# Optimization experiments

Hardware: AMD Instinct MI355X
Metric: run time of the kernel (lower is better)

## Reference

```python
import jax, jax.numpy as jnp
import numpy as np

HIDDEN = 2880
NUM_HEADS = 64
NUM_KV_HEADS = 8
HEAD_DIM = 64
ROPE_THETA = 150000.0
WINDOW = 128  # sliding window size (attend to last WINDOW tokens incl. current)
SCALE = HEAD_DIM ** -0.5
Q_SIZE = NUM_HEADS * HEAD_DIM          # 4096
KV_SIZE = NUM_KV_HEADS * HEAD_DIM      # 512


def _rope_neox(x, positions):
    # x: [T, n_heads, HEAD_DIM]; neox-style rotary over the full head dim
    half = HEAD_DIM // 2
    inv_freq = 1.0 / (ROPE_THETA ** (jnp.arange(half, dtype=jnp.float32) / half))
    freqs = positions.astype(jnp.float32)[:, None] * inv_freq[None, :]  # [T, half]
    cos = jnp.cos(freqs)[:, None, :]
    sin = jnp.sin(freqs)[:, None, :]
    x1, x2 = x[..., :half], x[..., half:]
    return jnp.concatenate([x1 * cos - x2 * sin, x2 * cos + x1 * sin], axis=-1)


def setup_inputs() -> dict:
    key = jax.random.key(0)
    k1, k2, k3, k4 = jax.random.split(key, 4)
    T = 2048
    hidden_states = jax.random.normal(k1, (T, HIDDEN), dtype=jnp.float32)
    positions = jnp.arange(T, dtype=jnp.int32)
    w_qkv = jax.random.normal(k2, (HIDDEN, Q_SIZE + 2 * KV_SIZE), dtype=jnp.float32) * (HIDDEN ** -0.5)
    w_o = jax.random.normal(k3, (Q_SIZE, HIDDEN), dtype=jnp.float32) * (Q_SIZE ** -0.5)
    sinks = jax.random.normal(k4, (NUM_HEADS,), dtype=jnp.float32)
    return {"positions": positions, "hidden_states": hidden_states,
            "w_qkv": w_qkv, "w_o": w_o, "sinks": sinks}


def reference(positions, hidden_states, w_qkv, w_o, sinks):
    T = hidden_states.shape[0]
    qkv = hidden_states @ w_qkv  # [T, 5120]
    q = qkv[:, :Q_SIZE].reshape(T, NUM_HEADS, HEAD_DIM)
    k = qkv[:, Q_SIZE:Q_SIZE + KV_SIZE].reshape(T, NUM_KV_HEADS, HEAD_DIM)
    v = qkv[:, Q_SIZE + KV_SIZE:].reshape(T, NUM_KV_HEADS, HEAD_DIM)

    q = _rope_neox(q, positions)
    k = _rope_neox(k, positions)

    # GQA: each group of NUM_HEADS//NUM_KV_HEADS query heads shares one kv head
    rep = NUM_HEADS // NUM_KV_HEADS
    k = jnp.repeat(k, rep, axis=1)  # [T, NUM_HEADS, HEAD_DIM]
    v = jnp.repeat(v, rep, axis=1)

    scores = jnp.einsum('qhd,khd->hqk', q, k) * SCALE  # [H, T, T]
    pos_q = positions[:, None]
    pos_k = positions[None, :]
    mask = (pos_k <= pos_q) & (pos_q - pos_k < WINDOW)  # causal + sliding window
    neg = jnp.finfo(scores.dtype).min
    scores = jnp.where(mask[None, :, :], scores, neg)

    # softmax with per-head learned sink logit included in the denominator
    m = jnp.maximum(scores.max(axis=-1), sinks[:, None])      # [H, T]
    e = jnp.exp(scores - m[..., None])                        # [H, T, T]
    denom = e.sum(axis=-1) + jnp.exp(sinks[:, None] - m)      # [H, T]
    probs = e / denom[..., None]

    attn = jnp.einsum('hqk,khd->qhd', probs, v).reshape(T, Q_SIZE)
    return attn @ w_o  # [T, HIDDEN]
```

## Files before the change

kernel.cpp:

```cpp
#include <hip/hip_runtime.h>
#include <hip/hip_bf16.h>

#define T_SEQ   2048
#define HIDDEN  2880
#define NQ      64
#define NKV     8
#define HD      64
#define QSIZE   4096
#define KVSIZE  512
#define QKV_N   5120
#define WINDOW  128
#define SCALE_F 0.125f
#define ROPE_L2 0.53733241958f

typedef unsigned short u16;
typedef __attribute__((ext_vector_type(8))) short short8;
typedef __attribute__((ext_vector_type(4))) float f32x4;

__device__ __forceinline__ u16 f2bf(float f) {
  __hip_bfloat16 b = __float2bfloat16(f);
  u16 u; __builtin_memcpy(&u, &b, 2); return u;
}

__device__ __forceinline__ void gload16(const u16* g, u16* l) {
  __builtin_amdgcn_global_load_lds(
      (const __attribute__((address_space(1))) void*)g,
      (__attribute__((address_space(3))) void*)l, 16, 0, 0);
}

#define CAST_BLKS 5760
#define TQ_BX 160
#define TQ_BLKS (160 * 45)
#define TO_BX 90
#define TO_BLKS (90 * 64)
#define PREP_BLKS (CAST_BLKS + TQ_BLKS + TO_BLKS)

__global__ void prep_kernel(const float* __restrict__ hidden,
                            const float* __restrict__ w_qkv,
                            const float* __restrict__ w_o,
                            u16* __restrict__ Xb, u16* __restrict__ Wqt,
                            u16* __restrict__ Wot) {
  __shared__ float tile[32][65];
  const int b = blockIdx.x, tid = threadIdx.x;
  if (b < CAST_BLKS) {
    int i = b * 256 + tid;
    float4 v = ((const float4*)hidden)[i];
    ushort4 o;
    o.x = f2bf(v.x); o.y = f2bf(v.y); o.z = f2bf(v.z); o.w = f2bf(v.w);
    ((ushort4*)Xb)[i] = o;
    return;
  }
  const float* in; u16* out; int R, C, bx, by;
  if (b < CAST_BLKS + TQ_BLKS) {
    int bb = b - CAST_BLKS; bx = bb % TQ_BX; by = bb / TQ_BX;
    in = w_qkv; out = Wqt; R = HIDDEN; C = QKV_N;
  } else {
    int bb = b - CAST_BLKS - TQ_BLKS; bx = bb % TO_BX; by = bb / TO_BX;
    in = w_o; out = Wot; R = QSIZE; C = HIDDEN;
  }
  const int r0 = by * 64, c0 = bx * 32;
  const int tx = tid & 31, ty = tid >> 5;
#pragma unroll
  for (int i = 0; i < 64; i += 8)
    tile[tx][ty + i] = in[(size_t)(r0 + ty + i) * C + c0 + tx];
  __syncthreads();
  const int tx2 = tid & 63, ty2 = tid >> 6;
#pragma unroll
  for (int i = 0; i < 32; i += 4)
    out[(size_t)(c0 + ty2 + i) * R + r0 + tx2] = f2bf(tile[ty2 + i][tx2]);
}

template <int MODE>
__global__ __launch_bounds__(256)
void gemm_bt_kernel(const u16* __restrict__ A, const u16* __restrict__ B,
                    float* __restrict__ Cout, const int* __restrict__ positions,
                    u16* __restrict__ qb, u16* __restrict__ kb,
                    u16* __restrict__ vb, int K, int Bvalid, int Nout, int ldc) {
  __shared__ __align__(16) u16 As[128 * 64];
  __shared__ __align__(16) u16 Bs[128 * 64];
  const int tid = threadIdx.x;
  const int lane = tid & 63, wave = tid >> 6;
  const int quad = lane >> 4, l16 = lane & 15;
  const int wm = wave >> 1, wn = wave & 1;
  const int m0 = blockIdx.x * 128, n0 = blockIdx.y * 128;

  const u16* Aptr[4]; const u16* Bptr[4]; u16* Alds[4]; u16* Blds[4];
#pragma unroll
  for (int it = 0; it < 4; ++it) {
    int c = it * 256 + tid;
    int r = c >> 3;
    int lcol = ((c & 7) ^ (r & 7)) * 8;
    Aptr[it] = A + (size_t)(m0 + r) * K + lcol;
    int br = n0 + r; br = br < Bvalid ? br : Bvalid - 1;
    Bptr[it] = B + (size_t)br * K + lcol;
    Alds[it] = As + c * 8;
    Blds[it] = Bs + c * 8;
  }

  f32x4 acc[4][4] = {};
  const int sw0 = (quad ^ (l16 & 7)) * 8;

  for (int kt = 0; kt < K; kt += 64) {
#pragma unroll
    for (int it = 0; it < 4; ++it) gload16(Aptr[it] + kt, Alds[it]);
#pragma unroll
    for (int it = 0; it < 4; ++it) gload16(Bptr[it] + kt, Blds[it]);
    asm volatile("s_waitcnt vmcnt(0)" ::: "memory");
    __syncthreads();
#pragma unroll
    for (int kk = 0; kk < 2; ++kk) {
      const int swo = sw0 ^ (kk * 32);
      short8 af[4], bf[4];
#pragma unroll
      for (int i = 0; i < 4; ++i)
        af[i] = *(const short8*)(As + (wm * 64 + i * 16 + l16) * 64 + swo);
#pragma unroll
      for (int j = 0; j < 4; ++j)
        bf[j] = *(const short8*)(Bs + (wn * 64 + j * 16 + l16) * 64 + swo);
#pragma unroll
      for (int i = 0; i < 4; ++i)
#pragma unroll
        for (int j = 0; j < 4; ++j)
          acc[i][j] = __builtin_amdgcn_mfma_f32_16x16x32_bf16(af[i], bf[j], acc[i][j], 0, 0, 0);
    }
    __syncthreads();
  }

  if (MODE == 0) {
#pragma unroll
    for (int i = 0; i < 4; ++i) {
      const int row = m0 + wm * 64 + i * 16 + quad * 4;
#pragma unroll
      for (int j = 0; j < 4; ++j) {
        const int col = n0 + wn * 64 + j * 16 + l16;
        if (col < Nout)
#pragma unroll
          for (int r = 0; r < 4; ++r)
            Cout[(size_t)(row + r) * ldc + col] = acc[i][j][r];
      }
    }
  } else {
    const int region = (n0 < QSIZE) ? 0 : (n0 < QSIZE + KVSIZE ? 1 : 2);
    if (region <= 1) {
      float invs[2];
#pragma unroll
      for (int j = 0; j < 2; ++j)
        invs[j] = exp2f(-(float)(j * 16 + l16) * ROPE_L2);
#pragma unroll
      for (int i = 0; i < 4; ++i) {
#pragma unroll
        for (int r = 0; r < 4; ++r) {
          const int row = m0 + wm * 64 + i * 16 + quad * 4 + r;
          const float pos = (float)positions[row];
#pragma unroll
          for (int j = 0; j < 2; ++j) {
            float s, c;
            sincosf(pos * invs[j], &s, &c);
            const float x1 = acc[i][j][r], x2 = acc[i][j + 2][r];
            const float o1 = x1 * c - x2 * s, o2 = x2 * c + x1 * s;
            const int col = n0 + wn * 64 + j * 16 + l16;
            if (region == 0) {
              qb[(size_t)row * QSIZE + col] = f2bf(o1);
              qb[(size_t)row * QSIZE + col + 32] = f2bf(o2);
            } else {
              kb[(size_t)row * KVSIZE + col - QSIZE] = f2bf(o1);
              kb[(size_t)row * KVSIZE + col - QSIZE + 32] = f2bf(o2);
            }
          }
        }
      }
    } else {
#pragma unroll
      for (int i = 0; i < 4; ++i) {
        const int row = m0 + wm * 64 + i * 16 + quad * 4;
#pragma unroll
        for (int j = 0; j < 4; ++j) {
          const int col = n0 + wn * 64 + j * 16 + l16 - (QSIZE + KVSIZE);
#pragma unroll
          for (int r = 0; r < 4; ++r)
            vb[(size_t)(row + r) * KVSIZE + col] = f2bf(acc[i][j][r]);
        }
      }
    }
  }
}

__global__ __launch_bounds__(256, 2)
void attn_kernel(const u16* __restrict__ qb, const u16* __restrict__ kb,
                 const u16* __restrict__ vb, const float* __restrict__ sinks,
                 u16* __restrict__ attnb) {
  __shared__ __align__(16) u16 Ks[160 * 72];
  __shared__ __align__(16) u16 Vt[64 * 164];
  __shared__ __align__(16) u16 Pb[4 * 16 * 164];
  const int qt = blockIdx.x, g = blockIdx.y;
  const int q0 = qt * 32, kstart = q0 - 128;
  const int tid = threadIdx.x;
  const int lane = tid & 63, wave = tid >> 6;
  const int quad = lane >> 4, l16 = lane & 15;

  for (int s = tid; s < 1280; s += 256) {
    int r = s >> 3, c8 = (s & 7) * 8;
    int tg = kstart + r; tg = tg < 0 ? 0 : tg;
    *(short8*)(Ks + r * 72 + c8) =
        *(const short8*)(kb + (size_t)tg * KVSIZE + g * HD + c8);
  }
  {
    const u16* vbase = vb + g * HD;
#pragma unroll
    for (int it = 0; it < 5; ++it) {
      int s = it * 256 + tid;
      int r = s >> 3, c8 = (s & 7) * 8;
      int tg = kstart + r; tg = tg < 0 ? 0 : tg;
      gload16(vbase + (size_t)tg * KVSIZE + c8, Pb + s * 8);
    }
  }
  asm volatile("s_waitcnt vmcnt(0)" ::: "memory");
  __syncthreads();

  short8 bk[10][2];
#pragma unroll
  for (int jf = 0; jf < 10; ++jf)
#pragma unroll
    for (int kk = 0; kk < 2; ++kk)
      bk[jf][kk] = *(const short8*)(Ks + (jf * 16 + l16) * 72 + kk * 32 + quad * 8);

  for (int s = tid; s < 1280; s += 256) {
    int k8 = s >> 6, d = s & 63;
    short8 tmp;
#pragma unroll
    for (int j = 0; j < 8; ++j) tmp[j] = (short)Pb[(k8 * 8 + j) * 64 + d];
    *(short8*)(Vt + d * 164 + k8 * 8) = tmp;
  }
  __syncthreads();

  const int strip = wave & 1, hb = wave >> 1;
  const int qrow0 = q0 + strip * 16;
  u16* Pw = Pb + wave * 16 * 164;
  for (int hh = 0; hh < 4; ++hh) {
    const int h = g * 8 + hb + hh * 2;
    short8 aq[2];
#pragma unroll
    for (int kk = 0; kk < 2; ++kk)
      aq[kk] = *(const short8*)(qb + (size_t)(qrow0 + l16) * QSIZE + h * HD + kk * 32 + quad * 8);
    f32x4 sc[10];
#pragma unroll
    for (int jf = 0; jf < 10; ++jf) {
      f32x4 c = {0.f, 0.f, 0.f, 0.f};
#pragma unroll
      for (int kk = 0; kk < 2; ++kk)
        c = __builtin_amdgcn_mfma_f32_16x16x32_bf16(aq[kk], bk[jf][kk], c, 0, 0, 0);
      sc[jf] = c;
    }

    const float sink = sinks[h];
    float pinv[4];
#pragma unroll
    for (int r = 0; r < 4; ++r) {
      const int qg = qrow0 + quad * 4 + r;
      float mx = -3.0e38f;
#pragma unroll
      for (int jf = 0; jf < 10; ++jf) {
        int kg = kstart + jf * 16 + l16;
        bool valid = (kg >= 0) && (kg <= qg) && (qg - kg < WINDOW);
        float sv = valid ? sc[jf][r] * SCALE_F : -3.0e38f;
        sc[jf][r] = sv;
        mx = fmaxf(mx, sv);
      }
#pragma unroll
      for (int d = 1; d < 16; d <<= 1) mx = fmaxf(mx, __shfl_xor(mx, d, 64));
      mx = fmaxf(mx, sink);
      float sum = 0.f;
#pragma unroll
      for (int jf = 0; jf < 10; ++jf) {
        float e = __expf(sc[jf][r] - mx);
        sc[jf][r] = e;
        sum += e;
      }
#pragma unroll
      for (int d = 1; d < 16; d <<= 1) sum += __shfl_xor(sum, d, 64);
      sum += __expf(sink - mx);
      pinv[r] = 1.0f / sum;
    }

#pragma unroll
    for (int jf = 0; jf < 10; ++jf)
#pragma unroll
      for (int r = 0; r < 4; ++r)
        Pw[(quad * 4 + r) * 164 + jf * 16 + l16] = f2bf(sc[jf][r] * pinv[r]);

    f32x4 o[4] = {};
#pragma unroll
    for (int kk = 0; kk < 5; ++kk) {
      short8 ap = *(const short8*)(Pw + l16 * 164 + kk * 32 + quad * 8);
#pragma unroll
      for (int jf = 0; jf < 4; ++jf) {
        short8 bv = *(const short8*)(Vt + (jf * 16 + l16) * 164 + kk * 32 + quad * 8);
        o[jf] = __builtin_amdgcn_mfma_f32_16x16x32_bf16(ap, bv, o[jf], 0, 0, 0);
      }
    }
#pragma unroll
    for (int jf = 0; jf < 4; ++jf)
#pragma unroll
      for (int r = 0; r < 4; ++r) {
        int qg = qrow0 + quad * 4 + r;
        attnb[(size_t)qg * QSIZE + h * HD + jf * 16 + l16] = f2bf(o[jf][r]);
      }
  }
}

extern "C" void kernel_launch(void* const* d_in, const int* in_sizes, int n_in,
                              void* d_out, int out_size, void* d_ws, size_t ws_size,
                              hipStream_t stream) {
  (void)in_sizes; (void)n_in; (void)out_size; (void)ws_size;
  const int*   positions = (const int*)d_in[0];
  const float* hidden    = (const float*)d_in[1];
  const float* w_qkv     = (const float*)d_in[2];
  const float* w_o       = (const float*)d_in[3];
  const float* sinks     = (const float*)d_in[4];

  char* p = (char*)d_ws;
  u16* Xb    = (u16*)p; p += (size_t)T_SEQ * HIDDEN * 2;
  u16* Wqt   = (u16*)p; p += (size_t)QKV_N * HIDDEN * 2;
  u16* Wot   = (u16*)p; p += (size_t)HIDDEN * QSIZE * 2;
  u16* qb    = (u16*)p; p += (size_t)T_SEQ * QSIZE * 2;
  u16* kb    = (u16*)p; p += (size_t)T_SEQ * KVSIZE * 2;
  u16* vb    = (u16*)p; p += (size_t)T_SEQ * KVSIZE * 2;
  u16* attnb = (u16*)p; p += (size_t)T_SEQ * QSIZE * 2;

  prep_kernel<<<PREP_BLKS, 256, 0, stream>>>(hidden, w_qkv, w_o, Xb, Wqt, Wot);
  gemm_bt_kernel<1><<<dim3(T_SEQ / 128, QKV_N / 128), 256, 0, stream>>>(
      Xb, Wqt, nullptr, positions, qb, kb, vb, HIDDEN, QKV_N, QKV_N, QKV_N);
  attn_kernel<<<dim3(T_SEQ / 32, NKV), 256, 0, stream>>>(qb, kb, vb, sinks, attnb);
  gemm_bt_kernel<0><<<dim3(T_SEQ / 128, 23), 256, 0, stream>>>(
      attnb, Wot, (float*)d_out, nullptr, nullptr, nullptr, nullptr,
      QSIZE, HIDDEN, HIDDEN, HIDDEN);
}
```

Baseline: 343.0 us.

## Double-buffer GEMM LDS tiles and remap blocks by XCD for L2 reuse

```diff
diff --git a/kernel.cpp b/kernel.cpp
--- a/kernel.cpp
+++ b/kernel.cpp
@@ -71,20 +71,28 @@
 }
 
 template <int MODE>
-__global__ __launch_bounds__(256)
+__global__ __launch_bounds__(256, 2)
 void gemm_bt_kernel(const u16* __restrict__ A, const u16* __restrict__ B,
                     float* __restrict__ Cout, const int* __restrict__ positions,
                     u16* __restrict__ qb, u16* __restrict__ kb,
-                    u16* __restrict__ vb, int K, int Bvalid, int Nout, int ldc) {
-  __shared__ __align__(16) u16 As[128 * 64];
-  __shared__ __align__(16) u16 Bs[128 * 64];
+                    u16* __restrict__ vb, int K, int NKT, int Bvalid, int Nout,
+                    int ldc, int NX, int NYC, int NY) {
+  __shared__ __align__(16) u16 As[2][128 * 64];
+  __shared__ __align__(16) u16 Bs[2][128 * 64];
+  const int bb = blockIdx.x;
+  const int xcd = bb & 7, bi = bb >> 3;
+  const int ny = xcd * NYC + (bi % NYC);
+  const int mx = bi / NYC;
+  if (ny >= NY || mx >= NX) return;
+  const int m0 = mx * 128, n0 = ny * 128;
+
   const int tid = threadIdx.x;
   const int lane = tid & 63, wave = tid >> 6;
   const int quad = lane >> 4, l16 = lane & 15;
   const int wm = wave >> 1, wn = wave & 1;
-  const int m0 = blockIdx.x * 128, n0 = blockIdx.y * 128;
-
-  const u16* Aptr[4]; const u16* Bptr[4]; u16* Alds[4]; u16* Blds[4];
+
+  const u16* Aptr[4]; const u16* Bptr[4];
+  u16* Al[2][4]; u16* Bl[2][4];
 #pragma unroll
   for (int it = 0; it < 4; ++it) {
     int c = it * 256 + tid;
@@ -93,37 +101,67 @@
     Aptr[it] = A + (size_t)(m0 + r) * K + lcol;
     int br = n0 + r; br = br < Bvalid ? br : Bvalid - 1;
     Bptr[it] = B + (size_t)br * K + lcol;
-    Alds[it] = As + c * 8;
-    Blds[it] = Bs + c * 8;
+    Al[0][it] = &As[0][c * 8]; Al[1][it] = &As[1][c * 8];
+    Bl[0][it] = &Bs[0][c * 8]; Bl[1][it] = &Bs[1][c * 8];
   }
 
   f32x4 acc[4][4] = {};
   const int sw0 = (quad ^ (l16 & 7)) * 8;
 
-  for (int kt = 0; kt < K; kt += 64) {
-#pragma unroll
-    for (int it = 0; it < 4; ++it) gload16(Aptr[it] + kt, Alds[it]);
-#pragma unroll
-    for (int it = 0; it < 4; ++it) gload16(Bptr[it] + kt, Blds[it]);
-    asm volatile("s_waitcnt vmcnt(0)" ::: "memory");
-    __syncthreads();
+#pragma unroll
+  for (int it = 0; it < 4; ++it) gload16(Aptr[it], Al[0][it]);
+#pragma unroll
+  for (int it = 0; it < 4; ++it) gload16(Bptr[it], Bl[0][it]);
+
+  int kt = 64;
+  for (int t = 0; t < NKT - 1; ++t, kt += 64) {
+    const int cur = t & 1, nxt = cur ^ 1;
+#pragma unroll
+    for (int it = 0; it < 4; ++it) gload16(Aptr[it] + kt, Al[nxt][it]);
+#pragma unroll
+    for (int it = 0; it < 4; ++it) gload16(Bptr[it] + kt, Bl[nxt][it]);
+    asm volatile("s_waitcnt vmcnt(8)\n\ts_barrier" ::: "memory");
+    const u16* Ab = &As[cur][0];
+    const u16* Bb = &Bs[cur][0];
 #pragma unroll
     for (int kk = 0; kk < 2; ++kk) {
       const int swo = sw0 ^ (kk * 32);
       short8 af[4], bf[4];
 #pragma unroll
       for (int i = 0; i < 4; ++i)
-        af[i] = *(const short8*)(As + (wm * 64 + i * 16 + l16) * 64 + swo);
+        af[i] = *(const short8*)(Ab + (wm * 64 + i * 16 + l16) * 64 + swo);
 #pragma unroll
       for (int j = 0; j < 4; ++j)
-        bf[j] = *(const short8*)(Bs + (wn * 64 + j * 16 + l16) * 64 + swo);
+        bf[j] = *(const short8*)(Bb + (wn * 64 + j * 16 + l16) * 64 + swo);
 #pragma unroll
       for (int i = 0; i < 4; ++i)
 #pragma unroll
         for (int j = 0; j < 4; ++j)
           acc[i][j] = __builtin_amdgcn_mfma_f32_16x16x32_bf16(af[i], bf[j], acc[i][j], 0, 0, 0);
     }
-    __syncthreads();
+    asm volatile("s_waitcnt lgkmcnt(0)\n\ts_barrier" ::: "memory");
+  }
+  {
+    const int cur = (NKT - 1) & 1;
+    asm volatile("s_waitcnt vmcnt(0)\n\ts_barrier" ::: "memory");
+    const u16* Ab = &As[cur][0];
+    const u16* Bb = &Bs[cur][0];
+#pragma unroll
+    for (int kk = 0; kk < 2; ++kk) {
+      const int swo = sw0 ^ (kk * 32);
+      short8 af[4], bf[4];
+#pragma unroll
+      for (int i = 0; i < 4; ++i)
+        af[i] = *(const short8*)(Ab + (wm * 64 + i * 16 + l16) * 64 + swo);
+#pragma unroll
+      for (int j = 0; j < 4; ++j)
+        bf[j] = *(const short8*)(Bb + (wn * 64 + j * 16 + l16) * 64 + swo);
+#pragma unroll
+      for (int i = 0; i < 4; ++i)
+#pragma unroll
+        for (int j = 0; j < 4; ++j)
+          acc[i][j] = __builtin_amdgcn_mfma_f32_16x16x32_bf16(af[i], bf[j], acc[i][j], 0, 0, 0);
+    }
   }
 
   if (MODE == 0) {
@@ -328,10 +366,11 @@
   u16* attnb = (u16*)p; p += (size_t)T_SEQ * QSIZE * 2;
 
   prep_kernel<<<PREP_BLKS, 256, 0, stream>>>(hidden, w_qkv, w_o, Xb, Wqt, Wot);
-  gemm_bt_kernel<1><<<dim3(T_SEQ / 128, QKV_N / 128), 256, 0, stream>>>(
-      Xb, Wqt, nullptr, positions, qb, kb, vb, HIDDEN, QKV_N, QKV_N, QKV_N);
+  gemm_bt_kernel<1><<<16 * 8 * 5, 256, 0, stream>>>(
+      Xb, Wqt, nullptr, positions, qb, kb, vb,
+      HIDDEN, 45, QKV_N, QKV_N, QKV_N, 16, 5, 40);
   attn_kernel<<<dim3(T_SEQ / 32, NKV), 256, 0, stream>>>(qb, kb, vb, sinks, attnb);
-  gemm_bt_kernel<0><<<dim3(T_SEQ / 128, 23), 256, 0, stream>>>(
+  gemm_bt_kernel<0><<<16 * 8 * 3, 256, 0, stream>>>(
       attnb, Wot, (float*)d_out, nullptr, nullptr, nullptr, nullptr,
-      QSIZE, HIDDEN, HIDDEN, HIDDEN);
-}
+      QSIZE, 64, HIDDEN, HIDDEN, HIDDEN, 16, 3, 23);
+}
```

After: 357.1 us. 1.04x slower.

## Split-K output GEMM with atomics, XCD-aware block mapping, vectorized weight transpose

Applied to the files above, without the earlier changes.

```diff
diff --git a/kernel.cpp b/kernel.cpp
--- a/kernel.cpp
+++ b/kernel.cpp
@@ -28,22 +28,28 @@
       (__attribute__((address_space(3))) void*)l, 16, 0, 0);
 }
 
+#define ZERO_BLKS 1440
 #define CAST_BLKS 5760
-#define TQ_BX 160
-#define TQ_BLKS (160 * 45)
-#define TO_BX 90
-#define TO_BLKS (90 * 64)
-#define PREP_BLKS (CAST_BLKS + TQ_BLKS + TO_BLKS)
+#define TQ_BX 80
+#define TQ_BLKS (80 * 45)
+#define TO_BX 45
+#define TO_BLKS (45 * 64)
+#define PREP_BLKS (ZERO_BLKS + CAST_BLKS + TQ_BLKS + TO_BLKS)
 
 __global__ void prep_kernel(const float* __restrict__ hidden,
                             const float* __restrict__ w_qkv,
                             const float* __restrict__ w_o,
                             u16* __restrict__ Xb, u16* __restrict__ Wqt,
-                            u16* __restrict__ Wot) {
-  __shared__ float tile[32][65];
+                            u16* __restrict__ Wot, float* __restrict__ dout) {
+  __shared__ float tile[64][65];
   const int b = blockIdx.x, tid = threadIdx.x;
-  if (b < CAST_BLKS) {
-    int i = b * 256 + tid;
+  if (b < ZERO_BLKS) {
+    float4 z = {0.f, 0.f, 0.f, 0.f};
+    ((float4*)dout)[(size_t)b * 256 + tid] = z;
+    return;
+  }
+  if (b < ZERO_BLKS + CAST_BLKS) {
+    size_t i = (size_t)(b - ZERO_BLKS) * 256 + tid;
     float4 v = ((const float4*)hidden)[i];
     ushort4 o;
     o.x = f2bf(v.x); o.y = f2bf(v.y); o.z = f2bf(v.z); o.w = f2bf(v.w);
@@ -51,23 +57,33 @@
     return;
   }
   const float* in; u16* out; int R, C, bx, by;
-  if (b < CAST_BLKS + TQ_BLKS) {
-    int bb = b - CAST_BLKS; bx = bb % TQ_BX; by = bb / TQ_BX;
+  if (b < ZERO_BLKS + CAST_BLKS + TQ_BLKS) {
+    int bb = b - ZERO_BLKS - CAST_BLKS; bx = bb % TQ_BX; by = bb / TQ_BX;
     in = w_qkv; out = Wqt; R = HIDDEN; C = QKV_N;
   } else {
-    int bb = b - CAST_BLKS - TQ_BLKS; bx = bb % TO_BX; by = bb / TO_BX;
+    int bb = b - ZERO_BLKS - CAST_BLKS - TQ_BLKS; bx = bb % TO_BX; by = bb / TO_BX;
     in = w_o; out = Wot; R = QSIZE; C = HIDDEN;
   }
-  const int r0 = by * 64, c0 = bx * 32;
-  const int tx = tid & 31, ty = tid >> 5;
-#pragma unroll
-  for (int i = 0; i < 64; i += 8)
-    tile[tx][ty + i] = in[(size_t)(r0 + ty + i) * C + c0 + tx];
+  const int r0 = by * 64, c0 = bx * 64;
+  const int tx = tid & 15, ty = tid >> 4;
+#pragma unroll
+  for (int i = 0; i < 4; ++i) {
+    float4 v = *(const float4*)(in + (size_t)(r0 + ty + 16 * i) * C + c0 + tx * 4);
+    tile[tx * 4 + 0][ty + 16 * i] = v.x;
+    tile[tx * 4 + 1][ty + 16 * i] = v.y;
+    tile[tx * 4 + 2][ty + 16 * i] = v.z;
+    tile[tx * 4 + 3][ty + 16 * i] = v.w;
+  }
   __syncthreads();
-  const int tx2 = tid & 63, ty2 = tid >> 6;
-#pragma unroll
-  for (int i = 0; i < 32; i += 4)
-    out[(size_t)(c0 + ty2 + i) * R + r0 + tx2] = f2bf(tile[ty2 + i][tx2]);
+  const int rr8 = (tid & 7) * 8, cc0 = tid >> 3;
+#pragma unroll
+  for (int p = 0; p < 2; ++p) {
+    int cc = cc0 + 32 * p;
+    short8 o;
+#pragma unroll
+    for (int j = 0; j < 8; ++j) o[j] = (short)f2bf(tile[cc][rr8 + j]);
+    *(short8*)(out + (size_t)(c0 + cc) * R + r0 + rr8) = o;
+  }
 }
 
 template <int MODE>
@@ -75,14 +91,22 @@
 void gemm_bt_kernel(const u16* __restrict__ A, const u16* __restrict__ B,
                     float* __restrict__ Cout, const int* __restrict__ positions,
                     u16* __restrict__ qb, u16* __restrict__ kb,
-                    u16* __restrict__ vb, int K, int Bvalid, int Nout, int ldc) {
+                    u16* __restrict__ vb, int Kstride, int NKT, int Ksplit,
+                    int Bvalid, int Nout, int ldc, int NX, int NYC, int NY) {
   __shared__ __align__(16) u16 As[128 * 64];
   __shared__ __align__(16) u16 Bs[128 * 64];
+  const int bb = blockIdx.x;
+  const int xcd = bb & 7, bi = bb >> 3;
+  const int ny = xcd * NYC + (bi % NYC);
+  const int mx = bi / NYC;
+  if (ny >= NY || mx >= NX) return;
+  const int m0 = mx * 128, n0 = ny * 128;
+  const int k0 = blockIdx.y * Ksplit;
+
   const int tid = threadIdx.x;
   const int lane = tid & 63, wave = tid >> 6;
   const int quad = lane >> 4, l16 = lane & 15;
   const int wm = wave >> 1, wn = wave & 1;
-  const int m0 = blockIdx.x * 128, n0 = blockIdx.y * 128;
 
   const u16* Aptr[4]; const u16* Bptr[4]; u16* Alds[4]; u16* Blds[4];
 #pragma unroll
@@ -90,9 +114,9 @@
     int c = it * 256 + tid;
     int r = c >> 3;
     int lcol = ((c & 7) ^ (r & 7)) * 8;
-    Aptr[it] = A + (size_t)(m0 + r) * K + lcol;
+    Aptr[it] = A + (size_t)(m0 + r) * Kstride + k0 + lcol;
     int br = n0 + r; br = br < Bvalid ? br : Bvalid - 1;
-    Bptr[it] = B + (size_t)br * K + lcol;
+    Bptr[it] = B + (size_t)br * Kstride + k0 + lcol;
     Alds[it] = As + c * 8;
     Blds[it] = Bs + c * 8;
   }
@@ -100,7 +124,7 @@
   f32x4 acc[4][4] = {};
   const int sw0 = (quad ^ (l16 & 7)) * 8;
 
-  for (int kt = 0; kt < K; kt += 64) {
+  for (int t = 0, kt = 0; t < NKT; ++t, kt += 64) {
 #pragma unroll
     for (int it = 0; it < 4; ++it) gload16(Aptr[it] + kt, Alds[it]);
 #pragma unroll
@@ -136,7 +160,7 @@
         if (col < Nout)
 #pragma unroll
           for (int r = 0; r < 4; ++r)
-            Cout[(size_t)(row + r) * ldc + col] = acc[i][j][r];
+            unsafeAtomicAdd(&Cout[(size_t)(row + r) * ldc + col], acc[i][j][r]);
       }
     }
   } else {
@@ -327,11 +351,13 @@
   u16* vb    = (u16*)p; p += (size_t)T_SEQ * KVSIZE * 2;
   u16* attnb = (u16*)p; p += (size_t)T_SEQ * QSIZE * 2;
 
-  prep_kernel<<<PREP_BLKS, 256, 0, stream>>>(hidden, w_qkv, w_o, Xb, Wqt, Wot);
-  gemm_bt_kernel<1><<<dim3(T_SEQ / 128, QKV_N / 128), 256, 0, stream>>>(
-      Xb, Wqt, nullptr, positions, qb, kb, vb, HIDDEN, QKV_N, QKV_N, QKV_N);
+  prep_kernel<<<PREP_BLKS, 256, 0, stream>>>(hidden, w_qkv, w_o, Xb, Wqt, Wot,
+                                             (float*)d_out);
+  gemm_bt_kernel<1><<<dim3(16 * 8 * 5, 1), 256, 0, stream>>>(
+      Xb, Wqt, nullptr, positions, qb, kb, vb,
+      HIDDEN, 45, 0, QKV_N, QKV_N, QKV_N, 16, 5, 40);
   attn_kernel<<<dim3(T_SEQ / 32, NKV), 256, 0, stream>>>(qb, kb, vb, sinks, attnb);
-  gemm_bt_kernel<0><<<dim3(T_SEQ / 128, 23), 256, 0, stream>>>(
+  gemm_bt_kernel<0><<<dim3(16 * 8 * 3, 2), 256, 0, stream>>>(
       attnb, Wot, (float*)d_out, nullptr, nullptr, nullptr, nullptr,
-      QSIZE, HIDDEN, HIDDEN, HIDDEN);
-}
+      QSIZE, 32, 2048, HIDDEN, HIDDEN, HIDDEN, 16, 3, 23);
+}
```

Result: slower. 366.7 us (+6.9%).
